# Kernel optimization log

Measured on AMD Instinct MI355X. Metric: run time of the kernel, lower is better.

The kernel has to match this reference:

```python
import jax, jax.numpy as jnp
import numpy as np

WINDOW = 16  # hardcoded in module __init__

B, S, E, H = 2, 2048, 1024, 16
HD = E // H


def setup_inputs() -> dict:
    key = jax.random.key(0)
    k1, k2, k3, k4, k5, k6 = jax.random.split(key, 6)
    input_embeddings = jax.random.normal(k1, (B, S, E), dtype=jnp.float32)
    token_ids = jax.random.randint(k2, (B, S), 0, 32000, dtype=jnp.int64)
    # nn.MultiheadAttention parameters: packed in_proj (3E, E) + bias, out_proj (E, E) + bias
    in_proj_weight = jax.random.normal(k3, (3 * E, E), dtype=jnp.float32) * 0.02
    in_proj_bias = jax.random.normal(k4, (3 * E,), dtype=jnp.float32) * 0.02
    out_proj_weight = jax.random.normal(k5, (E, E), dtype=jnp.float32) * 0.02
    out_proj_bias = jax.random.normal(k6, (E,), dtype=jnp.float32) * 0.02
    return {
        "input_embeddings": input_embeddings,
        "token_ids": token_ids,
        "in_proj_weight": in_proj_weight,
        "in_proj_bias": in_proj_bias,
        "out_proj_weight": out_proj_weight,
        "out_proj_bias": out_proj_bias,
    }


def _blocked_mask(seq_len: int) -> jnp.ndarray:
    # Module sets mask[i, j] = True for j in [i - WINDOW, i] (17 positions).
    # PyTorch bool attn_mask: True = NOT allowed to attend.
    i = jnp.arange(seq_len)[:, None]
    j = jnp.arange(seq_len)[None, :]
    return (j <= i) & (j >= i - WINDOW)  # [S, S] bool, True = masked out


def reference(input_embeddings, token_ids, in_proj_weight, in_proj_bias,
              out_proj_weight, out_proj_bias):
    x = input_embeddings  # [B, S, E]
    b, s, e = x.shape
    # Packed QKV projection (torch Linear: y = x W^T + b)
    qkv = jnp.einsum('bse,fe->bsf', x, in_proj_weight) + in_proj_bias  # [B, S, 3E]
    q, k, v = jnp.split(qkv, 3, axis=-1)
    # Split heads: [B, H, S, HD]
    q = q.reshape(b, s, H, HD).transpose(0, 2, 1, 3)
    k = k.reshape(b, s, H, HD).transpose(0, 2, 1, 3)
    v = v.reshape(b, s, H, HD).transpose(0, 2, 1, 3)
    scale = 1.0 / jnp.sqrt(jnp.asarray(HD, dtype=x.dtype))
    scores = jnp.einsum('bhqd,bhkd->bhqk', q * scale, k)  # [B, H, S, S]
    blocked = _blocked_mask(s)  # True = masked
    scores = jnp.where(blocked[None, None, :, :], -jnp.inf, scores)
    attn = jax.nn.softmax(scores, axis=-1)
    ctx = jnp.einsum('bhqk,bhkd->bhqd', attn, v)  # [B, H, S, HD]
    ctx = ctx.transpose(0, 2, 1, 3).reshape(b, s, e)
    out = jnp.einsum('bse,fe->bsf', ctx, out_proj_weight) + out_proj_bias
    return out
```

## Files before the change

kernel.cpp:

```cpp
#include <hip/hip_runtime.h>

typedef __attribute__((ext_vector_type(8))) __bf16 bf16x8;
typedef __attribute__((ext_vector_type(4))) float f32x4;
typedef unsigned short u16;
typedef unsigned int u32;

#define MFMA16(a, b, c) __builtin_amdgcn_mfma_f32_16x16x32_bf16((a), (b), (c), 0, 0, 0)

__device__ __forceinline__ u16 f2bf(float f) {
  u32 u = __float_as_uint(f);
  return (u16)((u + 0x7fffu + ((u >> 16) & 1u)) >> 16);
}

#define BDIM 2
#define SDIM 2048
#define EDIM 1024
#define HDIM 16
#define HD 64
#define MDIM (BDIM * SDIM)

#define SC_C1 0.1803368801111355f
#define SC_C2 4.328085122667252e+01f

#define SW(r) ((((r) & 3) ^ (((r) >> 2) & 3)))

typedef __attribute__((address_space(3))) void lds_void;
typedef __attribute__((address_space(1))) void g_void;

__device__ __forceinline__ void async_lds16(const void* g, void* lds_byte) {
  __builtin_amdgcn_global_load_lds((const g_void*)g, (lds_void*)lds_byte, 16, 0, 0);
}

__global__ __launch_bounds__(256) void cvt_kernel(const float* __restrict__ src,
                                                  u16* __restrict__ dst, int n) {
  int i = (blockIdx.x * 256 + threadIdx.x) * 8;
  if (i >= n) return;
  float4 f0 = *(const float4*)(src + i);
  float4 f1 = *(const float4*)(src + i + 4);
  union { uint4 u; u16 s[8]; } o;
  o.s[0] = f2bf(f0.x); o.s[1] = f2bf(f0.y); o.s[2] = f2bf(f0.z); o.s[3] = f2bf(f0.w);
  o.s[4] = f2bf(f1.x); o.s[5] = f2bf(f1.y); o.s[6] = f2bf(f1.z); o.s[7] = f2bf(f1.w);
  *(uint4*)(dst + i) = o.u;
}

__global__ __launch_bounds__(256) void gemm_qkv_kernel(
    const u16* __restrict__ X, const u16* __restrict__ W,
    const float* __restrict__ bias, u16* __restrict__ qb,
    u16* __restrict__ kb, u16* __restrict__ vtb) {
  __shared__ __align__(16) u16 As[128 * 32];
  __shared__ __align__(16) u16 Bs[128 * 32];
  const int m0 = blockIdx.x * 128, n0 = blockIdx.y * 128;
  const int t = threadIdx.x;
  const int l = t & 63;
  const int quad = l >> 4, col = l & 15;
  const int wid = t >> 6;
  const int mh = wid & 1, nh = wid >> 1;
  const int wofs = (t & 192) << 4;
  f32x4 acc[4][4] = {};
  const u16* Ab = X + (size_t)m0 * EDIM;
  const u16* Bb = W + (size_t)n0 * EDIM;
  char* AsB = (char*)As;
  char* BsB = (char*)Bs;

  for (int k0 = 0; k0 < EDIM; k0 += 32) {
    __syncthreads();
#pragma unroll
    for (int p = 0; p < 2; p++) {
      int idx = p * 256 + t;
      int row = idx >> 2;
      int kq = (idx & 3) ^ SW(row);
      async_lds16(Ab + (size_t)row * EDIM + k0 + kq * 8, AsB + p * 4096 + wofs);
      async_lds16(Bb + (size_t)row * EDIM + k0 + kq * 8, BsB + p * 4096 + wofs);
    }
    __syncthreads();
    bf16x8 af[4], bfr[4];
#pragma unroll
    for (int i = 0; i < 4; i++) {
      int ra = 64 * mh + 16 * i + col;
      af[i] = *(const bf16x8*)&As[(ra * 4 + (quad ^ SW(ra))) * 8];
      int rb = 64 * nh + 16 * i + col;
      bfr[i] = *(const bf16x8*)&Bs[(rb * 4 + (quad ^ SW(rb))) * 8];
    }
#pragma unroll
    for (int i = 0; i < 4; i++)
#pragma unroll
      for (int j = 0; j < 4; j++)
        acc[i][j] = MFMA16(af[i], bfr[j], acc[i][j]);
  }

#pragma unroll
  for (int i = 0; i < 4; i++)
#pragma unroll
    for (int j = 0; j < 4; j++)
#pragma unroll
      for (int r = 0; r < 4; r++) {
        int m = m0 + 64 * mh + 16 * i + quad * 4 + r;
        int n = n0 + 64 * nh + 16 * j + col;
        float val = acc[i][j][r] + bias[n];
        int which = n >> 10, e = n & 1023;
        int hh = e >> 6, d = e & 63;
        int bb = m >> 11, s = m & 2047;
        u16 bv = f2bf(val);
        size_t hb = (size_t)(bb * HDIM + hh);
        if (which == 0)
          qb[(hb * SDIM + s) * HD + d] = bv;
        else if (which == 1)
          kb[(hb * SDIM + s) * HD + d] = bv;
        else
          vtb[(hb * HD + d) * SDIM + s] = bv;
      }
}

__global__ __launch_bounds__(256) void attn_kernel(
    const u16* __restrict__ qg, const u16* __restrict__ kg,
    const u16* __restrict__ vtg, u16* __restrict__ ctx) {
  __shared__ __align__(16) u16 Ks[64 * 64];
  __shared__ __align__(16) u16 Vs[64 * 64];
  __shared__ __align__(16) u16 Ps[64 * 68];

  const int bh = blockIdx.x;
  const int q0 = blockIdx.y * 64;
  const int t = threadIdx.x;
  const int wid = t >> 6, l = t & 63;
  const int quad = l >> 4, col = l & 15;
  const size_t base = (size_t)bh * SDIM * HD;

  bf16x8 aq[2];
  {
    const u16* qp = qg + base + (size_t)(q0 + 16 * wid + col) * HD + quad * 8;
    aq[0] = *(const bf16x8*)(qp);
    aq[1] = *(const bf16x8*)(qp + 32);
  }
  const int qrow = q0 + 16 * wid + quad * 4;

  const int srow = t >> 3;
  const int g = (t & 7) ^ (srow & 7);
  const u16* kptr = kg + base + (size_t)srow * HD + g * 8;
  const u16* vptr = vtg + base + (size_t)srow * SDIM + g * 8;
  char* ldsK = (char*)Ks + ((t & 192) << 4);
  char* ldsV = (char*)Vs + ((t & 192) << 4);

  float psum[4] = {0.f, 0.f, 0.f, 0.f};
  f32x4 oacc[4] = {};

  for (int kt = 0; kt < SDIM / 64; kt++) {
    const int k0 = kt * 64;
    __syncthreads();
    async_lds16(kptr + (size_t)k0 * HD, ldsK);
    async_lds16(kptr + (size_t)(k0 + 32) * HD, ldsK + 4096);
    async_lds16(vptr + k0, ldsV);
    async_lds16(vptr + (size_t)32 * SDIM + k0, ldsV + 4096);
    __syncthreads();

    f32x4 sc[4] = {};
#pragma unroll
    for (int half = 0; half < 2; half++)
#pragma unroll
      for (int ct = 0; ct < 4; ct++) {
        int r = 16 * ct + col;
        int phys = (4 * half + quad) ^ (r & 7);
        bf16x8 bfrag = *(const bf16x8*)&Ks[r * 64 + phys * 8];
        sc[ct] = MFMA16(aq[half], bfrag, sc[ct]);
      }

    const int pbase = (16 * wid + quad * 4) * 68 + col;
    if (k0 <= q0 + 63 && k0 + 63 >= q0 - 16) {
#pragma unroll
      for (int ct = 0; ct < 4; ct++)
#pragma unroll
        for (int r = 0; r < 4; r++) {
          int i = qrow + r, j = k0 + 16 * ct + col;
          float arg = sc[ct][r] * SC_C1 - SC_C2;
          arg = (j <= i && j + 16 >= i) ? -1.0e30f : arg;
          float p = __builtin_exp2f(arg);
          psum[r] += p;
          Ps[pbase + r * 68 + 16 * ct] = f2bf(p);
        }
    } else {
#pragma unroll
      for (int ct = 0; ct < 4; ct++)
#pragma unroll
        for (int r = 0; r < 4; r++) {
          float p = __builtin_exp2f(sc[ct][r] * SC_C1 - SC_C2);
          psum[r] += p;
          Ps[pbase + r * 68 + 16 * ct] = f2bf(p);
        }
    }

#pragma unroll
    for (int half = 0; half < 2; half++) {
      bf16x8 pa = *(const bf16x8*)&Ps[(16 * wid + col) * 68 + half * 32 + quad * 8];
#pragma unroll
      for (int dt = 0; dt < 4; dt++) {
        int vr = 16 * dt + col;
        int phys = (4 * half + quad) ^ (vr & 7);
        bf16x8 vbf = *(const bf16x8*)&Vs[vr * 64 + phys * 8];
        oacc[dt] = MFMA16(pa, vbf, oacc[dt]);
      }
    }
  }

#pragma unroll
  for (int off = 1; off < 16; off <<= 1)
#pragma unroll
    for (int r = 0; r < 4; r++) psum[r] += __shfl_xor(psum[r], off, 64);

  const int b = bh >> 4, h = bh & 15;
  float linv[4];
#pragma unroll
  for (int r = 0; r < 4; r++) linv[r] = 1.0f / psum[r];
#pragma unroll
  for (int dt = 0; dt < 4; dt++)
#pragma unroll
    for (int r = 0; r < 4; r++) {
      int qgl = qrow + r;
      int d = 16 * dt + col;
      ctx[((size_t)(b * SDIM + qgl)) * EDIM + h * HD + d] =
          f2bf(oacc[dt][r] * linv[r]);
    }
}

__global__ __launch_bounds__(256) void gemm_out_kernel(
    const u16* __restrict__ A, const u16* __restrict__ W,
    const float* __restrict__ bias, float* __restrict__ out) {
  __shared__ __align__(16) u16 As[128 * 32];
  __shared__ __align__(16) u16 Bs[128 * 32];
  const int m0 = blockIdx.x * 128, n0 = blockIdx.y * 128;
  const int t = threadIdx.x;
  const int l = t & 63;
  const int quad = l >> 4, col = l & 15;
  const int wid = t >> 6;
  const int mh = wid & 1, nh = wid >> 1;
  const int wofs = (t & 192) << 4;
  f32x4 acc[4][4] = {};
  const u16* Ab = A + (size_t)m0 * EDIM;
  const u16* Bb = W + (size_t)n0 * EDIM;
  char* AsB = (char*)As;
  char* BsB = (char*)Bs;

  for (int k0 = 0; k0 < EDIM; k0 += 32) {
    __syncthreads();
#pragma unroll
    for (int p = 0; p < 2; p++) {
      int idx = p * 256 + t;
      int row = idx >> 2;
      int kq = (idx & 3) ^ SW(row);
      async_lds16(Ab + (size_t)row * EDIM + k0 + kq * 8, AsB + p * 4096 + wofs);
      async_lds16(Bb + (size_t)row * EDIM + k0 + kq * 8, BsB + p * 4096 + wofs);
    }
    __syncthreads();
    bf16x8 af[4], bfr[4];
#pragma unroll
    for (int i = 0; i < 4; i++) {
      int ra = 64 * mh + 16 * i + col;
      af[i] = *(const bf16x8*)&As[(ra * 4 + (quad ^ SW(ra))) * 8];
      int rb = 64 * nh + 16 * i + col;
      bfr[i] = *(const bf16x8*)&Bs[(rb * 4 + (quad ^ SW(rb))) * 8];
    }
#pragma unroll
    for (int i = 0; i < 4; i++)
#pragma unroll
      for (int j = 0; j < 4; j++)
        acc[i][j] = MFMA16(af[i], bfr[j], acc[i][j]);
  }

#pragma unroll
  for (int i = 0; i < 4; i++)
#pragma unroll
    for (int j = 0; j < 4; j++)
#pragma unroll
      for (int r = 0; r < 4; r++) {
        int m = m0 + 64 * mh + 16 * i + quad * 4 + r;
        int n = n0 + 64 * nh + 16 * j + col;
        out[(size_t)m * EDIM + n] = acc[i][j][r] + bias[n];
      }
}

extern "C" void kernel_launch(void* const* d_in, const int* in_sizes, int n_in,
                              void* d_out, int out_size, void* d_ws,
                              size_t ws_size, hipStream_t stream) {
  const float* x = (const float*)d_in[0];
  const float* in_w = (const float*)d_in[2];
  const float* in_b = (const float*)d_in[3];
  const float* out_w = (const float*)d_in[4];
  const float* out_b = (const float*)d_in[5];
  float* out = (float*)d_out;

  char* ws = (char*)d_ws;
  u16* Xb  = (u16*)ws;
  u16* ctx = (u16*)ws;
  u16* qb  = (u16*)(ws + (size_t)( 8 << 20));
  u16* kb  = (u16*)(ws + (size_t)(16 << 20));
  u16* vtb = (u16*)(ws + (size_t)(24 << 20));
  u16* Wib = (u16*)(ws + (size_t)(32 << 20));
  u16* Wob = (u16*)(ws + (size_t)(38 << 20));

  cvt_kernel<<<2048, 256, 0, stream>>>(x, Xb, MDIM * EDIM);
  cvt_kernel<<<1536, 256, 0, stream>>>(in_w, Wib, 3 * EDIM * EDIM);
  cvt_kernel<<<512, 256, 0, stream>>>(out_w, Wob, EDIM * EDIM);

  gemm_qkv_kernel<<<dim3(MDIM / 128, 3 * EDIM / 128), 256, 0, stream>>>(
      Xb, Wib, in_b, qb, kb, vtb);
  attn_kernel<<<dim3(BDIM * HDIM, SDIM / 64), 256, 0, stream>>>(qb, kb, vtb, ctx);
  gemm_out_kernel<<<dim3(MDIM / 128, EDIM / 128), 256, 0, stream>>>(
      ctx, Wob, out_b, out);
}
```

Before: 241.0 us.

## Pipeline attention K/V loads, fold scale into Q, fuse conversions, coalesce V stores

Fuses the three fp32-to-bf16 conversion launches into one kernel and uses a simpler round-half-up conversion. The QKV GEMM now pre-scales Q by the softmax constant, which removes the fixed max-offset subtraction. V tiles are computed transposed so the V^T stores are contiguous along the sequence. The attention loop double-buffers K and triple-buffers V with async LDS loads, and computes the next tile's QK^T ahead of the current softmax/PV step to overlap loads with compute. Dropping the constant offset risks exp2 overflow for large scores, and the extra buffers raise LDS use.

```diff
diff --git a/kernel.cpp b/kernel.cpp
--- a/kernel.cpp
+++ b/kernel.cpp
@@ -8,8 +8,7 @@
 #define MFMA16(a, b, c) __builtin_amdgcn_mfma_f32_16x16x32_bf16((a), (b), (c), 0, 0, 0)
 
 __device__ __forceinline__ u16 f2bf(float f) {
-  u32 u = __float_as_uint(f);
-  return (u16)((u + 0x7fffu + ((u >> 16) & 1u)) >> 16);
+  return (u16)((__float_as_uint(f) + 0x8000u) >> 16);
 }
 
 #define BDIM 2
@@ -20,7 +19,6 @@
 #define MDIM (BDIM * SDIM)
 
 #define SC_C1 0.1803368801111355f
-#define SC_C2 4.328085122667252e+01f
 
 #define SW(r) ((((r) & 3) ^ (((r) >> 2) & 3)))
 
@@ -31,16 +29,28 @@
   __builtin_amdgcn_global_load_lds((const g_void*)g, (lds_void*)lds_byte, 16, 0, 0);
 }
 
-__global__ __launch_bounds__(256) void cvt_kernel(const float* __restrict__ src,
-                                                  u16* __restrict__ dst, int n) {
+__global__ __launch_bounds__(256) void cvt3_kernel(
+    const float* __restrict__ s0, u16* __restrict__ d0, int n0,
+    const float* __restrict__ s1, u16* __restrict__ d1, int n1,
+    const float* __restrict__ s2, u16* __restrict__ d2, int n2) {
   int i = (blockIdx.x * 256 + threadIdx.x) * 8;
-  if (i >= n) return;
-  float4 f0 = *(const float4*)(src + i);
-  float4 f1 = *(const float4*)(src + i + 4);
-  union { uint4 u; u16 s[8]; } o;
-  o.s[0] = f2bf(f0.x); o.s[1] = f2bf(f0.y); o.s[2] = f2bf(f0.z); o.s[3] = f2bf(f0.w);
-  o.s[4] = f2bf(f1.x); o.s[5] = f2bf(f1.y); o.s[6] = f2bf(f1.z); o.s[7] = f2bf(f1.w);
-  *(uint4*)(dst + i) = o.u;
+  const float* s;
+  u16* d;
+  if (i < n0) {
+    s = s0 + i; d = d0 + i;
+  } else if (i < n0 + n1) {
+    s = s1 + (i - n0); d = d1 + (i - n0);
+  } else if (i < n0 + n1 + n2) {
+    s = s2 + (i - n0 - n1); d = d2 + (i - n0 - n1);
+  } else {
+    return;
+  }
+  float4 f0 = *(const float4*)(s);
+  float4 f1 = *(const float4*)(s + 4);
+  union { uint4 u; u16 h[8]; } o;
+  o.h[0] = f2bf(f0.x); o.h[1] = f2bf(f0.y); o.h[2] = f2bf(f0.z); o.h[3] = f2bf(f0.w);
+  o.h[4] = f2bf(f1.x); o.h[5] = f2bf(f1.y); o.h[6] = f2bf(f1.z); o.h[7] = f2bf(f1.w);
+  *(uint4*)(d) = o.u;
 }
 
 __global__ __launch_bounds__(256) void gemm_qkv_kernel(
@@ -50,6 +60,7 @@
   __shared__ __align__(16) u16 As[128 * 32];
   __shared__ __align__(16) u16 Bs[128 * 32];
   const int m0 = blockIdx.x * 128, n0 = blockIdx.y * 128;
+  const bool isV = (n0 >= 2 * EDIM);
   const int t = threadIdx.x;
   const int l = t & 63;
   const int quad = l >> 4, col = l & 15;
@@ -81,41 +92,61 @@
       int rb = 64 * nh + 16 * i + col;
       bfr[i] = *(const bf16x8*)&Bs[(rb * 4 + (quad ^ SW(rb))) * 8];
     }
+    if (isV) {
+#pragma unroll
+      for (int i = 0; i < 4; i++)
+#pragma unroll
+        for (int j = 0; j < 4; j++)
+          acc[i][j] = MFMA16(bfr[i], af[j], acc[i][j]);
+    } else {
+#pragma unroll
+      for (int i = 0; i < 4; i++)
+#pragma unroll
+        for (int j = 0; j < 4; j++)
+          acc[i][j] = MFMA16(af[i], bfr[j], acc[i][j]);
+    }
+  }
+
+  if (isV) {
 #pragma unroll
     for (int i = 0; i < 4; i++)
 #pragma unroll
       for (int j = 0; j < 4; j++)
-        acc[i][j] = MFMA16(af[i], bfr[j], acc[i][j]);
-  }
-
-#pragma unroll
-  for (int i = 0; i < 4; i++)
-#pragma unroll
-    for (int j = 0; j < 4; j++)
-#pragma unroll
-      for (int r = 0; r < 4; r++) {
-        int m = m0 + 64 * mh + 16 * i + quad * 4 + r;
-        int n = n0 + 64 * nh + 16 * j + col;
-        float val = acc[i][j][r] + bias[n];
-        int which = n >> 10, e = n & 1023;
-        int hh = e >> 6, d = e & 63;
-        int bb = m >> 11, s = m & 2047;
-        u16 bv = f2bf(val);
-        size_t hb = (size_t)(bb * HDIM + hh);
-        if (which == 0)
-          qb[(hb * SDIM + s) * HD + d] = bv;
-        else if (which == 1)
-          kb[(hb * SDIM + s) * HD + d] = bv;
-        else
-          vtb[(hb * HD + d) * SDIM + s] = bv;
-      }
+#pragma unroll
+        for (int r = 0; r < 4; r++) {
+          int n = n0 + 64 * nh + 16 * i + quad * 4 + r;
+          int m = m0 + 64 * mh + 16 * j + col;
+          float val = acc[i][j][r] + bias[n];
+          int e = n & 1023;
+          int hh = e >> 6, d = e & 63;
+          int bb = m >> 11, s = m & 2047;
+          vtb[(((size_t)(bb * HDIM + hh)) * HD + d) * SDIM + s] = f2bf(val);
+        }
+  } else {
+    const float qscale = (n0 < EDIM) ? SC_C1 : 1.0f;
+#pragma unroll
+    for (int i = 0; i < 4; i++)
+#pragma unroll
+      for (int j = 0; j < 4; j++)
+#pragma unroll
+        for (int r = 0; r < 4; r++) {
+          int m = m0 + 64 * mh + 16 * i + quad * 4 + r;
+          int n = n0 + 64 * nh + 16 * j + col;
+          float val = (acc[i][j][r] + bias[n]) * qscale;
+          int which = n >> 10, e = n & 1023;
+          int hh = e >> 6, d = e & 63;
+          int bb = m >> 11, s = m & 2047;
+          u16* dst = (which == 0) ? qb : kb;
+          dst[(((size_t)(bb * HDIM + hh)) * SDIM + s) * HD + d] = f2bf(val);
+        }
+  }
 }
 
 __global__ __launch_bounds__(256) void attn_kernel(
     const u16* __restrict__ qg, const u16* __restrict__ kg,
     const u16* __restrict__ vtg, u16* __restrict__ ctx) {
-  __shared__ __align__(16) u16 Ks[64 * 64];
-  __shared__ __align__(16) u16 Vs[64 * 64];
+  __shared__ __align__(16) u16 KB[2][64 * 64];
+  __shared__ __align__(16) u16 VB[3][64 * 64];
   __shared__ __align__(16) u16 Ps[64 * 68];
 
   const int bh = blockIdx.x;
@@ -137,32 +168,57 @@
   const int g = (t & 7) ^ (srow & 7);
   const u16* kptr = kg + base + (size_t)srow * HD + g * 8;
   const u16* vptr = vtg + base + (size_t)srow * SDIM + g * 8;
-  char* ldsK = (char*)Ks + ((t & 192) << 4);
-  char* ldsV = (char*)Vs + ((t & 192) << 4);
-
-  float psum[4] = {0.f, 0.f, 0.f, 0.f};
-  f32x4 oacc[4] = {};
-
-  for (int kt = 0; kt < SDIM / 64; kt++) {
-    const int k0 = kt * 64;
-    __syncthreads();
-    async_lds16(kptr + (size_t)k0 * HD, ldsK);
-    async_lds16(kptr + (size_t)(k0 + 32) * HD, ldsK + 4096);
-    async_lds16(vptr + k0, ldsV);
-    async_lds16(vptr + (size_t)32 * SDIM + k0, ldsV + 4096);
-    __syncthreads();
-
-    f32x4 sc[4] = {};
+  const int wofs = (t & 192) << 4;
+
+  auto stageK = [&](int kt, int buf) {
+    char* d = (char*)KB[buf] + wofs;
+    async_lds16(kptr + (size_t)(kt * 64) * HD, d);
+    async_lds16(kptr + (size_t)(kt * 64 + 32) * HD, d + 4096);
+  };
+  auto stageV = [&](int kt, int buf) {
+    char* d = (char*)VB[buf] + wofs;
+    async_lds16(vptr + kt * 64, d);
+    async_lds16(vptr + (size_t)32 * SDIM + kt * 64, d + 4096);
+  };
+  auto qkt = [&](const u16* Kt, f32x4* sco) {
 #pragma unroll
     for (int half = 0; half < 2; half++)
 #pragma unroll
       for (int ct = 0; ct < 4; ct++) {
         int r = 16 * ct + col;
         int phys = (4 * half + quad) ^ (r & 7);
-        bf16x8 bfrag = *(const bf16x8*)&Ks[r * 64 + phys * 8];
-        sc[ct] = MFMA16(aq[half], bfrag, sc[ct]);
+        bf16x8 bfrag = *(const bf16x8*)&Kt[r * 64 + phys * 8];
+        sco[ct] = MFMA16(aq[half], bfrag, sco[ct]);
       }
-
+  };
+
+  float psum[4] = {};
+  f32x4 oacc[4] = {};
+  f32x4 sc[4] = {}, scn[4];
+
+  const int NT = SDIM / 64;
+  stageK(0, 0);
+  stageV(0, 0);
+  __syncthreads();
+  qkt(KB[0], sc);
+  stageK(1, 1);
+  stageV(1, 1);
+
+  int vb_n = 2;
+  for (int kt = 0; kt < NT; kt++) {
+    __syncthreads();
+    if (kt + 1 < NT) {
+#pragma unroll
+      for (int ct = 0; ct < 4; ct++) scn[ct] = f32x4{0.f, 0.f, 0.f, 0.f};
+      qkt(KB[(kt + 1) & 1], scn);
+    }
+    if (kt + 2 < NT) {
+      stageK(kt + 2, kt & 1);
+      stageV(kt + 2, vb_n);
+    }
+    vb_n = (vb_n == 2) ? 0 : vb_n + 1;
+
+    const int k0 = kt * 64;
     const int pbase = (16 * wid + quad * 4) * 68 + col;
     if (k0 <= q0 + 63 && k0 + 63 >= q0 - 16) {
 #pragma unroll
@@ -170,8 +226,7 @@
 #pragma unroll
         for (int r = 0; r < 4; r++) {
           int i = qrow + r, j = k0 + 16 * ct + col;
-          float arg = sc[ct][r] * SC_C1 - SC_C2;
-          arg = (j <= i && j + 16 >= i) ? -1.0e30f : arg;
+          float arg = (j <= i && j + 16 >= i) ? -1.0e30f : sc[ct][r];
           float p = __builtin_exp2f(arg);
           psum[r] += p;
           Ps[pbase + r * 68 + 16 * ct] = f2bf(p);
@@ -181,23 +236,27 @@
       for (int ct = 0; ct < 4; ct++)
 #pragma unroll
         for (int r = 0; r < 4; r++) {
-          float p = __builtin_exp2f(sc[ct][r] * SC_C1 - SC_C2);
+          float p = __builtin_exp2f(sc[ct][r]);
           psum[r] += p;
           Ps[pbase + r * 68 + 16 * ct] = f2bf(p);
         }
     }
 
+    const u16* Vt = VB[kt % 3];
 #pragma unroll
     for (int half = 0; half < 2; half++) {
-      bf16x8 pa = *(const bf16x8*)&Ps[(16 * wid + col) * 68 + half * 32 + quad * 8];
+      bf16x8 pa =
+          *(const bf16x8*)&Ps[(16 * wid + col) * 68 + half * 32 + quad * 8];
 #pragma unroll
       for (int dt = 0; dt < 4; dt++) {
         int vr = 16 * dt + col;
         int phys = (4 * half + quad) ^ (vr & 7);
-        bf16x8 vbf = *(const bf16x8*)&Vs[vr * 64 + phys * 8];
+        bf16x8 vbf = *(const bf16x8*)&Vt[vr * 64 + phys * 8];
         oacc[dt] = MFMA16(pa, vbf, oacc[dt]);
       }
     }
+#pragma unroll
+    for (int ct = 0; ct < 4; ct++) sc[ct] = scn[ct];
   }
 
 #pragma unroll
@@ -295,9 +354,11 @@
   u16* Wib = (u16*)(ws + (size_t)(32 << 20));
   u16* Wob = (u16*)(ws + (size_t)(38 << 20));
 
-  cvt_kernel<<<2048, 256, 0, stream>>>(x, Xb, MDIM * EDIM);
-  cvt_kernel<<<1536, 256, 0, stream>>>(in_w, Wib, 3 * EDIM * EDIM);
-  cvt_kernel<<<512, 256, 0, stream>>>(out_w, Wob, EDIM * EDIM);
+  const int nX = MDIM * EDIM;
+  const int nWi = 3 * EDIM * EDIM;
+  const int nWo = EDIM * EDIM;
+  cvt3_kernel<<<(nX + nWi + nWo) / 8 / 256, 256, 0, stream>>>(
+      x, Xb, nX, in_w, Wib, nWi, out_w, Wob, nWo);
 
   gemm_qkv_kernel<<<dim3(MDIM / 128, 3 * EDIM / 128), 256, 0, stream>>>(
       Xb, Wib, in_b, qb, kb, vtb);
```

After: 222.6 us. -7.6%, faster.
